# Kernel optimization log

Hardware: AMD Instinct MI355X
Metric: run time of the kernel (lower is better)

The kernel has to match this reference:

```python
import jax, jax.numpy as jnp
import numpy as np

N, E, B = 100000, 1600000, 64
TD, VD, AD = 768, 2048, 512
HC, H = 32, 4
NV, NA = 20000, 20000


def setup_inputs() -> dict:
    key = jax.random.key(0)
    ks = iter(jax.random.split(key, 80))
    def nrm(shape, scale=0.05):
        return (jax.random.normal(next(ks), shape, jnp.float32) * scale)
    inp = {}
    inp["x"] = jax.random.normal(next(ks), (N, TD), jnp.float32)
    inp["x_vision"] = jax.random.normal(next(ks), (NV, VD), jnp.float32)
    inp["x_audio"] = jax.random.normal(next(ks), (NA, AD), jnp.float32)
    inp["src"] = jax.random.randint(next(ks), (E,), 0, N, jnp.int32)
    inp["dst"] = jax.random.randint(next(ks), (E,), 0, N, jnp.int32)
    inp["vidx"] = jnp.arange(NV, dtype=jnp.int32) + 1000   # disjoint vision node ids
    inp["aidx"] = jnp.arange(NA, dtype=jnp.int32) + 30000  # disjoint audio node ids
    inp["ptr"] = (jnp.arange(B + 1) * (N // B)).astype(jnp.int32)
    # modality projections
    inp["Wt"] = nrm((HC, TD)); inp["bt"] = jnp.zeros((HC,), jnp.float32)
    inp["Wv"] = nrm((HC, VD)); inp["bv"] = jnp.zeros((HC,), jnp.float32)
    inp["gv"] = jnp.ones((HC,), jnp.float32); inp["bev"] = jnp.zeros((HC,), jnp.float32)
    inp["Wa"] = nrm((HC, AD)); inp["ba"] = jnp.zeros((HC,), jnp.float32)
    inp["ga"] = jnp.ones((HC,), jnp.float32); inp["bea"] = jnp.zeros((HC,), jnp.float32)
    # GATv2 convs: (in_dim, heads, concat)
    for p, cin, h, concat in (("c1", HC, H, True), ("c2", HC * H, H, True), ("c3", HC * H, H, True), ("c4", HC * H, 1, False)):
        inp[p + "_Wl"] = nrm((h * HC, cin)); inp[p + "_bl"] = jnp.zeros((h * HC,), jnp.float32)
        inp[p + "_Wr"] = nrm((h * HC, cin)); inp[p + "_br"] = jnp.zeros((h * HC,), jnp.float32)
        inp[p + "_att"] = nrm((h, HC))
        inp[p + "_b"] = jnp.zeros((h * HC if concat else HC,), jnp.float32)
    # layer norms
    for p, d in (("n1", HC * H), ("n2", HC * H), ("n3", HC * H), ("n4", HC)):
        inp[p + "_g"] = jnp.ones((d,), jnp.float32); inp[p + "_b"] = jnp.zeros((d,), jnp.float32)
    inp["Wo"] = nrm((1, HC), 0.01); inp["bo"] = jnp.zeros((1,), jnp.float32)
    return inp


def layernorm(x, g, b):
    m = x.mean(-1, keepdims=True)
    v = x.var(-1, keepdims=True)
    return (x - m) / jnp.sqrt(v + 1e-5) * g + b


def gatv2(x, src, dst, Wl, bl, Wr, br, att, b, concat):
    # PyG GATv2Conv (share_weights=False): e = att . leaky_relu(xl[src] + xr[dst])
    n = x.shape[0]
    h, c = att.shape
    xl = (x @ Wl.T + bl).reshape(n, h, c)
    xr = (x @ Wr.T + br).reshape(n, h, c)
    e = jnp.einsum('ehc,hc->eh', jax.nn.leaky_relu(xl[src] + xr[dst], 0.2), att)
    m = jax.ops.segment_max(e, dst, num_segments=n)          # segment softmax over dst
    w = jnp.exp(e - m[dst])
    s = jax.ops.segment_sum(w, dst, num_segments=n)
    alpha = w / (s[dst] + 1e-16)
    out = jax.ops.segment_sum(alpha[:, :, None] * xl[src], dst, num_segments=n)
    out = out.reshape(n, h * c) if concat else out.mean(1)
    return out + b


def reference(x, x_vision, x_audio, Wt, bt, Wv, bv, gv, bev, Wa, ba, ga, bea,
              c1_Wl, c1_bl, c1_Wr, c1_br, c1_att, c1_b,
              c2_Wl, c2_bl, c2_Wr, c2_br, c2_att, c2_b,
              c3_Wl, c3_bl, c3_Wr, c3_br, c3_att, c3_b,
              c4_Wl, c4_bl, c4_Wr, c4_br, c4_att, c4_b,
              n1_g, n1_b, n2_g, n2_b, n3_g, n3_b, n4_g, n4_b, Wo, bo,
              src, dst, vidx, aidx, ptr):
    n = x.shape[0]
    sl = jnp.arange(n, dtype=src.dtype)  # add_self_loops=True
    s2 = jnp.concatenate([src, sl]); d2 = jnp.concatenate([dst, sl])
    fx = x @ Wt.T + bt  # text projection (dropout = identity in eval)
    hv = jax.nn.relu(layernorm(x_vision @ Wv.T + bv, gv, bev))
    fx = fx.at[vidx].set(hv * x[vidx].mean(1, keepdims=True))
    ha = jax.nn.relu(layernorm(x_audio @ Wa.T + ba, ga, bea))
    fx = fx.at[aidx].set(ha * x[aidx].mean(1, keepdims=True))
    h1 = jax.nn.elu(layernorm(gatv2(fx, s2, d2, c1_Wl, c1_bl, c1_Wr, c1_br, c1_att, c1_b, True), n1_g, n1_b))
    h2 = jax.nn.elu(layernorm(gatv2(h1, s2, d2, c2_Wl, c2_bl, c2_Wr, c2_br, c2_att, c2_b, True) + h1, n2_g, n2_b))
    h3 = jax.nn.elu(layernorm(gatv2(h2, s2, d2, c3_Wl, c3_bl, c3_Wr, c3_br, c3_att, c3_b, True) + h2, n3_g, n3_b))
    h4 = layernorm(gatv2(h3, s2, d2, c4_Wl, c4_bl, c4_Wr, c4_br, c4_att, c4_b, False), n4_g, n4_b)
    summary = h4[ptr[:-1]]  # summary node = first node of each graph
    out = (summary @ Wo.T + bo).squeeze(-1)  # num_classes==2 -> squeeze
    return out
```

## Files before the change

kernel.cpp:

```cpp
#include <hip/hip_runtime.h>
#include <math.h>

#define NND 100000
#define NED 1600000
#define TDIM 768
#define VDIM 2048
#define ADIM 512
#define NVV 20000
#define NAA 20000
#define NBB 64
#define SUBROWS 8192

#define NBLK_N ((NND + 255) / 256)
#define NBLK_E ((NED + 255) / 256)
#define NSCAN ((NND + 1023) / 1024)
#define NPACK 576
#define NTB_TXT (NND / 32)
#define NTB_VIS (NVV / 32)
#define NTB_AUD (NAA / 32)

static __device__ __forceinline__ unsigned short f2bf(float f) {
  unsigned int u = __float_as_uint(f);
  unsigned int r = (u + 0x7fffu + ((u >> 16) & 1u)) >> 16;
  return (unsigned short)r;
}
static __device__ __forceinline__ float bf2f(unsigned int s) {
  return __uint_as_float(s << 16);
}

typedef __attribute__((ext_vector_type(8))) short bfrag;
typedef __attribute__((ext_vector_type(4))) float facc4;

static __device__ __forceinline__ bfrag pack8(const float4& a, const float4& b) {
  union { bfrag v; unsigned short u[8]; } r;
  r.u[0] = f2bf(a.x); r.u[1] = f2bf(a.y); r.u[2] = f2bf(a.z); r.u[3] = f2bf(a.w);
  r.u[4] = f2bf(b.x); r.u[5] = f2bf(b.y); r.u[6] = f2bf(b.z); r.u[7] = f2bf(b.w);
  return r.v;
}

static __device__ __forceinline__ float red16(float v) {
  #pragma unroll
  for (int m = 8; m >= 1; m >>= 1) v += __shfl_xor(v, m, 64);
  return v;
}
static __device__ __forceinline__ float red32(float v) {
  #pragma unroll
  for (int m = 16; m >= 1; m >>= 1) v += __shfl_xor(v, m, 64);
  return v;
}

__global__ void k_init(int* cnt, int* fill, int* m3, int* m2, int* cnts, int* agg, int n) {
  int i = blockIdx.x * 256 + threadIdx.x;
  if (i < n) { cnt[i] = 1; fill[i] = 1; m3[i] = 0; m2[i] = 0; }
  if (i < 2) cnts[i] = 0;
  if (i < 128) agg[i] = 0;
}

__global__ void k_cntpack(
    const int* __restrict__ dst, int* cnt,
    const float* __restrict__ W0l, const float* __restrict__ W0r, unsigned short* o0,
    const float* __restrict__ W1l, const float* __restrict__ W1r, unsigned short* o1,
    const float* __restrict__ W2l, const float* __restrict__ W2r, unsigned short* o2,
    const float* __restrict__ W3l, const float* __restrict__ W3r, unsigned short* o3,
    const float* __restrict__ Wt, unsigned short* ot,
    const float* __restrict__ Wv, unsigned short* ov,
    const float* __restrict__ Wa, unsigned short* oa) {
  int bid = blockIdx.x;
  if (bid < NBLK_E) {
    int i = bid * 256 + threadIdx.x;
    if (i < NED) atomicAdd(&cnt[dst[i]], 1);
    return;
  }
  int i = (bid - NBLK_E) * 256 + threadIdx.x;
  if (i < 4096) { o0[i] = f2bf(W0l[i]); o0[4096 + i] = f2bf(W0r[i]); return; }
  i -= 4096;
  if (i < 16384) { o1[i] = f2bf(W1l[i]); o1[16384 + i] = f2bf(W1r[i]); return; }
  i -= 16384;
  if (i < 16384) { o2[i] = f2bf(W2l[i]); o2[16384 + i] = f2bf(W2r[i]); return; }
  i -= 16384;
  if (i < 4096) { o3[i] = f2bf(W3l[i]); o3[4096 + i] = f2bf(W3r[i]); return; }
  i -= 4096;
  if (i < 24576) { ot[i] = f2bf(Wt[i]); return; }
  i -= 24576;
  if (i < 65536) { ov[i] = f2bf(Wv[i]); return; }
  i -= 65536;
  if (i < 16384) { oa[i] = f2bf(Wa[i]); return; }
}

__global__ void k_scanall(const int* __restrict__ cnt, int* rp, int* agg, int n) {
  __shared__ int lds[256];
  int t = threadIdx.x, b = blockIdx.x;
  int base = b * 1024;
  int v[4];
  int s = 0;
  #pragma unroll
  for (int j = 0; j < 4; ++j) {
    int i = base + t * 4 + j;
    int c = (i < n) ? cnt[i] : 0;
    s += c; v[j] = s;
  }
  lds[t] = s;
  __syncthreads();
  for (int ofs = 1; ofs < 256; ofs <<= 1) {
    int x = (t >= ofs) ? lds[t - ofs] : 0;
    __syncthreads();
    lds[t] += x;
    __syncthreads();
  }
  int excl = (t > 0) ? lds[t - 1] : 0;
  int total = lds[255];
  if (t == 0) atomicExch(&agg[b], total);
  __syncthreads();
  int psum = 0;
  for (int j = t; j < b; j += 256) {
    int a;
    do { a = atomicAdd(&agg[j], 0); } while (a == 0);
    psum += a;
  }
  lds[t] = psum;
  __syncthreads();
  for (int ofs = 128; ofs >= 1; ofs >>= 1) {
    if (t < ofs) lds[t] += lds[t + ofs];
    __syncthreads();
  }
  int prefix = lds[0];
  #pragma unroll
  for (int j = 0; j < 4; ++j) {
    int i = base + t * 4 + j;
    if (i < n) rp[i + 1] = prefix + excl + v[j];
  }
  if (b == 0 && t == 0) rp[0] = 0;
}

__global__ void k_fill(const int* __restrict__ src, const int* __restrict__ dst,
                       const int* __restrict__ rp, int* fill, int* colidx, int n, int e) {
  int i = blockIdx.x * 256 + threadIdx.x;
  if (i < n) colidx[rp[i]] = i;
  if (i < e) {
    int d = dst[i];
    int p = atomicAdd(&fill[d], 1);
    colidx[rp[d] + p] = src[i];
  }
}

__global__ void k_prep4m(const int* __restrict__ ptr, const int* __restrict__ rp,
                         const int* __restrict__ colidx, int* off, int* gidx, int* mark3) {
  if (blockIdx.x > 0) {
    int node = ptr[blockIdx.x - 1];
    int eb = rp[node], ee = rp[node + 1];
    if (threadIdx.x == 0) mark3[node] = 1;
    for (int e = eb + (int)threadIdx.x; e < ee; e += 256) mark3[colidx[e]] = 1;
    return;
  }
  __shared__ int cnt_s[64];
  __shared__ int off_s[65];
  int t = threadIdx.x;
  if (t < 64) {
    int node = ptr[t];
    int deg = rp[node + 1] - rp[node];
    if (deg > 126) deg = 126;
    cnt_s[t] = deg + 1;
  }
  __syncthreads();
  if (t == 0) {
    int acc = 0;
    for (int i = 0; i < 64; ++i) { off_s[i] = acc; acc += cnt_s[i]; }
    off_s[64] = acc;
  }
  __syncthreads();
  if (t < 65) off[t] = off_s[t];
  if (t < 64) {
    int node = ptr[t];
    int o = off_s[t];
    gidx[o] = node;
    int eb = rp[node];
    int deg = cnt_s[t] - 1;
    for (int j = 0; j < deg; ++j) gidx[o + 1 + j] = colidx[eb + j];
  }
}

__global__ void k_mark2s(const int* __restrict__ mark3, const int* __restrict__ rp,
                         const int* __restrict__ colidx, int* mark2, int n) {
  int i = blockIdx.x * 256 + threadIdx.x;
  if (i >= n || !mark3[i]) return;
  mark2[i] = 1;
  int eb = rp[i], ee = rp[i + 1];
  for (int e = eb; e < ee; ++e) mark2[colidx[e]] = 1;
}

__global__ void k_compact2(const int* __restrict__ m3, const int* __restrict__ m2,
                           int* l3, int* l2, int* cnts, int n) {
  int i = blockIdx.x * 256 + threadIdx.x;
  if (i < n) {
    if (m3[i]) { int p = atomicAdd(&cnts[0], 1); l3[p] = i; }
    if (m2[i]) { int p = atomicAdd(&cnts[1], 1); l2[p] = i; }
  }
}

template <int K, bool MEAN, bool OBF>
static __device__ __forceinline__ void gemm_in_body(
    const float* __restrict__ A, const unsigned short* __restrict__ Wb,
    const float* __restrict__ bias, void* __restrict__ Cv,
    float* __restrict__ rowmean, int bid, float* lred) {
  constexpr int KH = K / 2;
  constexpr int KT2 = KH / 32;
  constexpr int NG = KT2 / 2;
  static_assert(KT2 % 2 == 0 && NG % 2 == 0, "need even group count");
  const int wid = (int)threadIdx.x >> 6;
  const int lane = (int)threadIdx.x & 63;
  const int tile = wid & 1;
  const int kh = wid >> 1;
  const int r16 = lane & 15;
  const int kg = lane >> 4;
  const int m0 = (bid * 2 + tile) * 16;
  const float* arow = A + (size_t)(m0 + r16) * K + kh * KH + kg * 8;
  const unsigned short* w0 = Wb + (size_t)r16 * K + kh * KH + kg * 8;
  const unsigned short* w1 = Wb + (size_t)(16 + r16) * K + kh * KH + kg * 8;

  float4 A0[4], A1[4];
  bfrag W0[4], W1[4];
  facc4 acc0 = (facc4){0.f, 0.f, 0.f, 0.f};
  facc4 acc1 = (facc4){0.f, 0.f, 0.f, 0.f};
  float msum = 0.f;

  auto loadg = [&](float4* dA, bfrag* dW, int g) {
    #pragma unroll
    for (int t = 0; t < 2; ++t) {
      const float4* ap = reinterpret_cast<const float4*>(arow + (g * 2 + t) * 32);
      dA[2 * t] = ap[0];
      dA[2 * t + 1] = ap[1];
    }
    #pragma unroll
    for (int t = 0; t < 2; ++t) {
      dW[2 * t]     = *reinterpret_cast<const bfrag*>(w0 + (g * 2 + t) * 32);
      dW[2 * t + 1] = *reinterpret_cast<const bfrag*>(w1 + (g * 2 + t) * 32);
    }
  };
  auto consume = [&](const float4* sA, const bfrag* sW) {
    #pragma unroll
    for (int t = 0; t < 2; ++t) {
      float4 a0 = sA[2 * t], a1 = sA[2 * t + 1];
      if (MEAN) msum += (a0.x + a0.y + a0.z + a0.w) + (a1.x + a1.y + a1.z + a1.w);
      bfrag af = pack8(a0, a1);
      acc0 = __builtin_amdgcn_mfma_f32_16x16x32_bf16(af, sW[2 * t], acc0, 0, 0, 0);
      acc1 = __builtin_amdgcn_mfma_f32_16x16x32_bf16(af, sW[2 * t + 1], acc1, 0, 0, 0);
    }
  };

  loadg(A0, W0, 0);
  #pragma unroll 1
  for (int g = 0; g < NG; g += 2) {
    loadg(A1, W1, g + 1);
    __builtin_amdgcn_sched_barrier(0);
    consume(A0, W0);
    if (g + 2 < NG) loadg(A0, W0, g + 2);
    __builtin_amdgcn_sched_barrier(0);
    consume(A1, W1);
  }

  float* my = lred + ((size_t)tile * 64 + lane) * 9;
  if (kh == 1) {
    #pragma unroll
    for (int r = 0; r < 4; ++r) { my[r] = acc0[r]; my[4 + r] = acc1[r]; }
    my[8] = msum;
  }
  __syncthreads();
  if (kh == 1) return;
  #pragma unroll
  for (int r = 0; r < 4; ++r) { acc0[r] += my[r]; acc1[r] += my[4 + r]; }
  if (MEAN) msum += my[8];

  float b0v = bias[r16], b1v = bias[16 + r16];
  #pragma unroll
  for (int r = 0; r < 4; ++r) {
    int rowg = m0 + kg * 4 + r;
    float v0 = acc0[r] + b0v, v1 = acc1[r] + b1v;
    if (OBF) {
      unsigned short* C = (unsigned short*)Cv;
      C[(size_t)rowg * 32 + r16] = f2bf(v0);
      C[(size_t)rowg * 32 + 16 + r16] = f2bf(v1);
    } else {
      float* C = (float*)Cv;
      C[(size_t)rowg * 32 + r16] = v0;
      C[(size_t)rowg * 32 + 16 + r16] = v1;
    }
  }
  if (MEAN) {
    msum += __shfl_xor(msum, 16, 64);
    msum += __shfl_xor(msum, 32, 64);
    if (lane < 16) rowmean[m0 + r16] = msum * (1.f / (float)K);
  }
}

__global__ __launch_bounds__(256) void k_gemm_in_all(
    const float* __restrict__ x, const unsigned short* __restrict__ wbt,
    const float* __restrict__ bt, unsigned short* fx, float* rowmean,
    const float* __restrict__ xv, const unsigned short* __restrict__ wbv,
    const float* __restrict__ bv, float* hvraw,
    const float* __restrict__ xa, const unsigned short* __restrict__ wba,
    const float* __restrict__ ba, float* haraw) {
  __shared__ float lred[2 * 64 * 9];
  int bid = blockIdx.x;
  if (bid < NTB_TXT) {
    gemm_in_body<TDIM, true, true>(x, wbt, bt, fx, rowmean, bid, lred);
  } else if (bid < NTB_TXT + NTB_VIS) {
    gemm_in_body<VDIM, false, false>(xv, wbv, bv, hvraw, nullptr, bid - NTB_TXT, lred);
  } else {
    gemm_in_body<ADIM, false, false>(xa, wba, ba, haraw, nullptr, bid - NTB_TXT - NTB_VIS, lred);
  }
}

template <int K, int NHALF, int WAVES, int MODE>
__global__ __launch_bounds__(WAVES * 64) void gemm_mfma(
    const unsigned short* __restrict__ A,
    const unsigned short* __restrict__ Wb,
    const float* __restrict__ bl, const float* __restrict__ br,
    unsigned short* __restrict__ Cl, unsigned short* __restrict__ Cr, int M,
    const int* __restrict__ rows, const int* __restrict__ rcnt) {
  constexpr int KT = K / 32;
  constexpr int NT = 2 * NHALF / 16;
  constexpr int NPW = NT / WAVES;
  static_assert(NPW >= 1, "bad wave split");
  const int wid = (int)threadIdx.x >> 6;
  const int lane = (int)threadIdx.x & 63;
  const int r16 = lane & 15;
  const int kg = lane >> 4;
  const int m0 = blockIdx.x * 16;
  int nr = M;
  if (MODE >= 1) nr = *rcnt;
  if (m0 >= nr) return;
  bfrag bf[NPW][KT];
  #pragma unroll
  for (int n = 0; n < NPW; ++n) {
    int col = (wid * NPW + n) * 16 + r16;
    #pragma unroll
    for (int kt = 0; kt < KT; ++kt)
      bf[n][kt] = *reinterpret_cast<const bfrag*>(Wb + (size_t)col * K + kt * 32 + kg * 8);
  }
  int ra = m0 + r16;
  if (MODE >= 1) { int mm = ra < nr ? ra : nr - 1; ra = rows[mm]; }
  bfrag af[KT];
  const unsigned short* arow = A + (size_t)ra * K + kg * 8;
  #pragma unroll
  for (int kt = 0; kt < KT; ++kt)
    af[kt] = *reinterpret_cast<const bfrag*>(arow + kt * 32);
  facc4 acc[NPW];
  #pragma unroll
  for (int n = 0; n < NPW; ++n) acc[n] = (facc4){0.f, 0.f, 0.f, 0.f};
  #pragma unroll
  for (int kt = 0; kt < KT; ++kt)
    #pragma unroll
    for (int n = 0; n < NPW; ++n)
      acc[n] = __builtin_amdgcn_mfma_f32_16x16x32_bf16(af[kt], bf[n][kt], acc[n], 0, 0, 0);
  #pragma unroll
  for (int n = 0; n < NPW; ++n) {
    int colg = (wid * NPW + n) * 16 + r16;
    bool isL = colg < NHALF;
    float bias = isL ? bl[colg] : br[colg - NHALF];
    #pragma unroll
    for (int r = 0; r < 4; ++r) {
      int m = m0 + kg * 4 + r;
      if (MODE == 1 && m >= nr) continue;
      int rowg = (MODE == 1) ? rows[m] : m;
      unsigned short v = f2bf(acc[n][r] + bias);
      if (isL) Cl[(size_t)rowg * NHALF + colg] = v;
      else     Cr[(size_t)rowg * NHALF + (colg - NHALF)] = v;
    }
  }
}

template <bool RES, bool WL>
__global__ __launch_bounds__(256) void gat_agg_post128(
    const unsigned short* __restrict__ xl, const unsigned short* __restrict__ xr,
    const float* __restrict__ att,
    const int* __restrict__ rp, const int* __restrict__ colidx,
    const float* __restrict__ cb, const unsigned short* res,
    const float* __restrict__ g, const float* __restrict__ b,
    unsigned short* __restrict__ out, int n,
    const int* __restrict__ wl, const int* __restrict__ wcnt) {
  int wid = (blockIdx.x * 256 + threadIdx.x) >> 6;
  int node;
  if (WL) {
    if (wid >= *wcnt) return;
    node = wl[wid];
  } else {
    if (wid >= n) return;
    node = wid;
  }
  const int base = node * 128;
  int l = threadIdx.x & 63;
  const int lh = l & 31;
  const int half = l >> 5;
  const int c4 = 4 * lh;
  float4 a = *reinterpret_cast<const float4*>(att + c4);
  uint2 xru = *reinterpret_cast<const uint2*>(xr + base + c4);
  float xr0 = bf2f(xru.x & 0xffffu), xr1 = bf2f(xru.x >> 16);
  float xr2 = bf2f(xru.y & 0xffffu), xr3 = bf2f(xru.y >> 16);
  float m_ = -1e30f, s_ = 0.f;
  float ac0 = 0.f, ac1 = 0.f, ac2 = 0.f, ac3 = 0.f;
  int eb = rp[node], ee = rp[node + 1];
  int cnt = ee - eb;
  int nstep = (cnt + 1) >> 1;

  auto step = [&](uint2 cur, bool go) {
    float x0 = bf2f(cur.x & 0xffffu), x1 = bf2f(cur.x >> 16);
    float x2 = bf2f(cur.y & 0xffffu), x3 = bf2f(cur.y >> 16);
    float z0 = x0 + xr0, z1 = x1 + xr1, z2 = x2 + xr2, z3 = x3 + xr3;
    float t = (z0 > 0.f ? z0 : 0.2f * z0) * a.x + (z1 > 0.f ? z1 : 0.2f * z1) * a.y
            + (z2 > 0.f ? z2 : 0.2f * z2) * a.z + (z3 > 0.f ? z3 : 0.2f * z3) * a.w;
    t += __shfl_xor(t, 1, 64);
    t += __shfl_xor(t, 2, 64);
    t += __shfl_xor(t, 4, 64);
    if (!go) t = -1e30f;
    if (__any(t > m_ + 4.0f)) {
      float nm = fmaxf(m_, t);
      float p = __expf(m_ - nm);
      float w = __expf(t - nm);
      s_ = s_ * p + w;
      ac0 = ac0 * p + w * x0; ac1 = ac1 * p + w * x1;
      ac2 = ac2 * p + w * x2; ac3 = ac3 * p + w * x3;
      m_ = nm;
    } else {
      float w = __expf(t - m_);
      s_ += w;
      ac0 = fmaf(w, x0, ac0); ac1 = fmaf(w, x1, ac1);
      ac2 = fmaf(w, x2, ac2); ac3 = fmaf(w, x3, ac3);
    }
  };
  auto eclamp = [&](int s) { int e = 2 * s + half; return eb + (e < cnt ? e : cnt - 1); };
  auto ldx = [&](int sn) {
    return *reinterpret_cast<const uint2*>(xl + (size_t)sn * 128 + c4);
  };

  int idx[4];
  uint2 pv[4];
  #pragma unroll
  for (int k = 0; k < 4; ++k) idx[k] = colidx[eclamp(k)];
  #pragma unroll
  for (int k = 0; k < 4; ++k) pv[k] = ldx(idx[k]);
  for (int i = 0; i < nstep; i += 4) {
    uint2 q[4];
    #pragma unroll
    for (int k = 0; k < 4; ++k) q[k] = pv[k];
    if (i + 4 < nstep) {
      #pragma unroll
      for (int k = 0; k < 4; ++k) idx[k] = colidx[eclamp(i + 4 + k)];
      #pragma unroll
      for (int k = 0; k < 4; ++k) pv[k] = ldx(idx[k]);
    }
    step(q[0], 2 * i + half < cnt);
    if (i + 1 < nstep) step(q[1], 2 * (i + 1) + half < cnt);
    if (i + 2 < nstep) step(q[2], 2 * (i + 2) + half < cnt);
    if (i + 3 < nstep) step(q[3], 2 * (i + 3) + half < cnt);
  }

  float om = __shfl_xor(m_, 32, 64);
  float os = __shfl_xor(s_, 32, 64);
  float oa0 = __shfl_xor(ac0, 32, 64);
  float oa1 = __shfl_xor(ac1, 32, 64);
  float oa2 = __shfl_xor(ac2, 32, 64);
  float oa3 = __shfl_xor(ac3, 32, 64);
  float nm = fmaxf(m_, om);
  float ps = __expf(m_ - nm), po = __expf(om - nm);
  float s = s_ * ps + os * po;
  float inv = 1.f / (s + 1e-16f);
  float4 cbv = *reinterpret_cast<const float4*>(cb + c4);
  float v0 = (ac0 * ps + oa0 * po) * inv + cbv.x;
  float v1 = (ac1 * ps + oa1 * po) * inv + cbv.y;
  float v2 = (ac2 * ps + oa2 * po) * inv + cbv.z;
  float v3 = (ac3 * ps + oa3 * po) * inv + cbv.w;
  if (RES) {
    uint2 rv = *reinterpret_cast<const uint2*>(res + base + c4);
    v0 += bf2f(rv.x & 0xffffu); v1 += bf2f(rv.x >> 16);
    v2 += bf2f(rv.y & 0xffffu); v3 += bf2f(rv.y >> 16);
  }
  float S = v0 + v1 + v2 + v3;
  float Q = v0 * v0 + v1 * v1 + v2 * v2 + v3 * v3;
  #pragma unroll
  for (int m = 16; m >= 1; m >>= 1) {
    S += __shfl_xor(S, m, 64);
    Q += __shfl_xor(Q, m, 64);
  }
  float mean = S * (1.f / 128.f);
  float var = Q * (1.f / 128.f) - mean * mean;
  float rstd = rsqrtf(var + 1e-5f);
  float4 gv = *reinterpret_cast<const float4*>(g + c4);
  float4 bv = *reinterpret_cast<const float4*>(b + c4);
  float y0 = (v0 - mean) * rstd * gv.x + bv.x;
  float y1 = (v1 - mean) * rstd * gv.y + bv.y;
  float y2 = (v2 - mean) * rstd * gv.z + bv.z;
  float y3 = (v3 - mean) * rstd * gv.w + bv.w;
  y0 = (y0 > 0.f) ? y0 : expm1f(y0);
  y1 = (y1 > 0.f) ? y1 : expm1f(y1);
  y2 = (y2 > 0.f) ? y2 : expm1f(y2);
  y3 = (y3 > 0.f) ? y3 : expm1f(y3);
  if (half == 0) {
    uint2 o;
    o.x = (unsigned int)f2bf(y0) | ((unsigned int)f2bf(y1) << 16);
    o.y = (unsigned int)f2bf(y2) | ((unsigned int)f2bf(y3) << 16);
    *reinterpret_cast<uint2*>(out + base + c4) = o;
  }
}

__global__ __launch_bounds__(256) void k_agg4_final(
    const unsigned short* __restrict__ xls, const unsigned short* __restrict__ xrs,
    const float* __restrict__ att, const int* __restrict__ off,
    const float* __restrict__ cb, const float* __restrict__ g,
    const float* __restrict__ b, const float* __restrict__ Wo,
    const float* __restrict__ bo, float* __restrict__ out) {
  int wid = (blockIdx.x * 256 + threadIdx.x) >> 6;
  int l = threadIdx.x & 63;
  int lg = l & 15;
  int node = 4 * wid + (l >> 4);
  int c2 = 2 * lg;
  int p0 = off[node], pe = off[node + 1];
  int deg = pe - p0 - 1;
  float2 a = *reinterpret_cast<const float2*>(att + c2);
  unsigned int xru = *reinterpret_cast<const unsigned int*>(xrs + (size_t)p0 * 32 + c2);
  float xr0 = bf2f(xru & 0xffffu), xr1 = bf2f(xru >> 16);
  float m_ = -1e30f, s_ = 0.f, accx = 0.f, accy = 0.f;
  for (int i = 0;; ++i) {
    bool go = i < deg;
    if (!__any(go)) break;
    float xcx = 0.f, xcy = 0.f;
    float t = -1e30f;
    if (go) {
      unsigned int pv = *reinterpret_cast<const unsigned int*>(xls + (size_t)(p0 + 1 + i) * 32 + c2);
      xcx = bf2f(pv & 0xffffu);
      xcy = bf2f(pv >> 16);
      float z0 = xcx + xr0, z1 = xcy + xr1;
      t = (z0 > 0.f ? z0 : 0.2f * z0) * a.x + (z1 > 0.f ? z1 : 0.2f * z1) * a.y;
    }
    t = red16(t);
    if (!go) t = -1e30f;
    if (__any(t > m_ + 4.0f)) {
      float nm = fmaxf(m_, t);
      float p = __expf(m_ - nm);
      float w = __expf(t - nm);
      s_ = s_ * p + w;
      accx = accx * p + w * xcx;
      accy = accy * p + w * xcy;
      m_ = nm;
    } else {
      float w = __expf(t - m_);
      s_ += w;
      accx = fmaf(w, xcx, accx);
      accy = fmaf(w, xcy, accy);
    }
  }
  float inv = 1.f / (s_ + 1e-16f);
  float2 cbv = *reinterpret_cast<const float2*>(cb + c2);
  float v0 = accx * inv + cbv.x;
  float v1 = accy * inv + cbv.y;
  float S = red16(v0 + v1);
  float Q = red16(v0 * v0 + v1 * v1);
  float mean = S * (1.f / 32.f);
  float var = Q * (1.f / 32.f) - mean * mean;
  float rstd = rsqrtf(var + 1e-5f);
  float2 gv = *reinterpret_cast<const float2*>(g + c2);
  float2 bv = *reinterpret_cast<const float2*>(b + c2);
  float y0 = (v0 - mean) * rstd * gv.x + bv.x;
  float y1 = (v1 - mean) * rstd * gv.y + bv.y;
  float2 wo = *reinterpret_cast<const float2*>(Wo + c2);
  float d = red16(y0 * wo.x + y1 * wo.y);
  if (lg == 0) out[node] = d + bo[0];
}

__global__ __launch_bounds__(256) void k_modal2(
    unsigned short* fx, const float* __restrict__ hv, const float* __restrict__ ha,
    const int* __restrict__ vidx, const int* __restrict__ aidx,
    const float* __restrict__ gv, const float* __restrict__ bev,
    const float* __restrict__ ga, const float* __restrict__ bea,
    const float* __restrict__ rowmean, int nv, int na) {
  int wid = (blockIdx.x * 256 + threadIdx.x) >> 6;
  int l = threadIdx.x & 63;
  if (wid >= nv + na) return;
  bool isV = wid < nv;
  int w2 = isV ? wid : wid - nv;
  const float* hraw = isV ? hv : ha;
  const float* gg = isV ? gv : ga;
  const float* be = isV ? bev : bea;
  int node = isV ? vidx[w2] : aidx[w2];
  float mean = rowmean[node];
  float hval = (l < 32) ? hraw[(size_t)w2 * 32 + l] : 0.f;
  float S = red32(hval);
  float Q = red32(hval * hval);
  if (l < 32) {
    float m2 = S * (1.f / 32.f);
    float var = Q * (1.f / 32.f) - m2 * m2;
    float rstd = rsqrtf(var + 1e-5f);
    float y = (hval - m2) * rstd * gg[l] + be[l];
    y = fmaxf(y, 0.f);
    fx[(size_t)node * 32 + l] = f2bf(y * mean);
  }
}

extern "C" void kernel_launch(void* const* d_in, const int* in_sizes, int n_in,
                              void* d_out, int out_size, void* d_ws, size_t ws_size,
                              hipStream_t stream) {
  const float* x   = (const float*)d_in[0];
  const float* xv  = (const float*)d_in[1];
  const float* xa  = (const float*)d_in[2];
  const int* src   = (const int*)d_in[3];
  const int* dst   = (const int*)d_in[4];
  const int* vidx  = (const int*)d_in[5];
  const int* aidx  = (const int*)d_in[6];
  const int* ptr   = (const int*)d_in[7];
  const float* Wt  = (const float*)d_in[8];
  const float* bt  = (const float*)d_in[9];
  const float* Wv  = (const float*)d_in[10];
  const float* bv  = (const float*)d_in[11];
  const float* gv  = (const float*)d_in[12];
  const float* bev = (const float*)d_in[13];
  const float* Wa  = (const float*)d_in[14];
  const float* ba  = (const float*)d_in[15];
  const float* ga  = (const float*)d_in[16];
  const float* bea = (const float*)d_in[17];
  const float* cW_l[4], *cb_l[4], *cW_r[4], *cb_r[4], *c_att[4], *c_b[4];
  for (int i = 0; i < 4; ++i) {
    cW_l[i]  = (const float*)d_in[18 + 6 * i + 0];
    cb_l[i]  = (const float*)d_in[18 + 6 * i + 1];
    cW_r[i]  = (const float*)d_in[18 + 6 * i + 2];
    cb_r[i]  = (const float*)d_in[18 + 6 * i + 3];
    c_att[i] = (const float*)d_in[18 + 6 * i + 4];
    c_b[i]   = (const float*)d_in[18 + 6 * i + 5];
  }
  const float* ng[4], *nb_[4];
  for (int i = 0; i < 4; ++i) {
    ng[i]  = (const float*)d_in[42 + 2 * i + 0];
    nb_[i] = (const float*)d_in[42 + 2 * i + 1];
  }
  const float* Wo = (const float*)d_in[50];
  const float* bo = (const float*)d_in[51];
  float* out = (float*)d_out;

  char* w = (char*)d_ws;
  auto alloc = [&](size_t bytes) {
    char* p = w;
    w += (bytes + 255) & ~(size_t)255;
    return p;
  };
  int* rowptr = (int*)alloc((NND + 1) * sizeof(int));
  int* cnt    = (int*)alloc(NND * sizeof(int));
  int* aggs   = (int*)alloc(128 * sizeof(int));
  int* colidx = (int*)alloc((size_t)(NED + NND) * sizeof(int));
  float* rowmean = (float*)alloc((size_t)NND * sizeof(float));
  unsigned short* fx = (unsigned short*)alloc((size_t)NND * 32 * sizeof(unsigned short));
  unsigned short* h  = (unsigned short*)alloc((size_t)NND * 128 * sizeof(unsigned short));
  unsigned short* xlb = (unsigned short*)alloc((size_t)NND * 128 * sizeof(unsigned short));
  unsigned short* xrb = (unsigned short*)alloc((size_t)NND * 128 * sizeof(unsigned short));
  float* hvraw = (float*)alloc((size_t)NVV * 32 * sizeof(float));
  float* haraw = (float*)alloc((size_t)NAA * 32 * sizeof(float));
  unsigned short* wb0 = (unsigned short*)alloc(256 * 32 * sizeof(unsigned short));
  unsigned short* wb1 = (unsigned short*)alloc(256 * 128 * sizeof(unsigned short));
  unsigned short* wb2 = (unsigned short*)alloc(256 * 128 * sizeof(unsigned short));
  unsigned short* wb3 = (unsigned short*)alloc(64 * 128 * sizeof(unsigned short));
  unsigned short* wbt = (unsigned short*)alloc(32 * TDIM * sizeof(unsigned short));
  unsigned short* wbv = (unsigned short*)alloc(32 * VDIM * sizeof(unsigned short));
  unsigned short* wba = (unsigned short*)alloc(32 * ADIM * sizeof(unsigned short));
  int* off4 = (int*)alloc(65 * sizeof(int));
  int* gidx = (int*)alloc(SUBROWS * sizeof(int));
  unsigned short* xls = (unsigned short*)alloc((size_t)SUBROWS * 32 * sizeof(unsigned short));
  unsigned short* xrs = (unsigned short*)alloc((size_t)SUBROWS * 32 * sizeof(unsigned short));
  int* mark3 = (int*)alloc((size_t)NND * sizeof(int));
  int* mark2 = (int*)alloc((size_t)NND * sizeof(int));
  int* list3 = (int*)alloc((size_t)NND * sizeof(int));
  int* list2 = (int*)alloc((size_t)NND * sizeof(int));
  int* cnts  = (int*)alloc(2 * sizeof(int));

  const int nwave_n = (NND * 64 + 255) / 256;
  const int nwave_m2 = ((NVV + NAA) * 64 + 255) / 256;
  const int ntile = (NND + 15) / 16;

  int* fill = list2;
  k_init<<<NBLK_N, 256, 0, stream>>>(cnt, fill, mark3, mark2, cnts, aggs, NND);
  k_cntpack<<<NBLK_E + NPACK, 256, 0, stream>>>(
      dst, cnt,
      cW_l[0], cW_r[0], wb0, cW_l[1], cW_r[1], wb1,
      cW_l[2], cW_r[2], wb2, cW_l[3], cW_r[3], wb3,
      Wt, wbt, Wv, wbv, Wa, wba);
  k_scanall<<<NSCAN, 256, 0, stream>>>(cnt, rowptr, aggs, NND);
  k_fill<<<NBLK_E, 256, 0, stream>>>(src, dst, rowptr, fill, colidx, NND, NED);
  k_prep4m<<<65, 256, 0, stream>>>(ptr, rowptr, colidx, off4, gidx, mark3);
  k_mark2s<<<NBLK_N, 256, 0, stream>>>(mark3, rowptr, colidx, mark2, NND);
  k_compact2<<<NBLK_N, 256, 0, stream>>>(mark3, mark2, list3, list2, cnts, NND);
  k_gemm_in_all<<<NTB_TXT + NTB_VIS + NTB_AUD, 256, 0, stream>>>(
      x, wbt, bt, fx, rowmean, xv, wbv, bv, hvraw, xa, wba, ba, haraw);
  k_modal2<<<nwave_m2, 256, 0, stream>>>(
      fx, hvraw, haraw, vidx, aidx, gv, bev, ga, bea, rowmean, NVV, NAA);

  gemm_mfma<32, 128, 8, 0><<<ntile, 512, 0, stream>>>(
      fx, wb0, cb_l[0], cb_r[0], xlb, xrb, NND, nullptr, nullptr);
  gat_agg_post128<false, false><<<nwave_n, 256, 0, stream>>>(
      xlb, xrb, c_att[0], rowptr, colidx, c_b[0], nullptr, ng[0], nb_[0], h, NND,
      nullptr, nullptr);

  gemm_mfma<128, 128, 8, 0><<<ntile, 512, 0, stream>>>(
      h, wb1, cb_l[1], cb_r[1], xlb, xrb, NND, nullptr, nullptr);
  gat_agg_post128<true, true><<<nwave_n, 256, 0, stream>>>(
      xlb, xrb, c_att[1], rowptr, colidx, c_b[1], h, ng[1], nb_[1], h, NND,
      list2, cnts + 1);

  gemm_mfma<128, 128, 8, 1><<<ntile, 512, 0, stream>>>(
      h, wb2, cb_l[2], cb_r[2], xlb, xrb, NND, list2, cnts + 1);
  gat_agg_post128<true, true><<<4096, 256, 0, stream>>>(
      xlb, xrb, c_att[2], rowptr, colidx, c_b[2], h, ng[2], nb_[2], h, NND,
      list3, cnts + 0);

  gemm_mfma<128, 32, 4, 2><<<SUBROWS / 16, 256, 0, stream>>>(
      h, wb3, cb_l[3], cb_r[3], xls, xrs, SUBROWS, gidx, off4 + 64);
  k_agg4_final<<<4, 256, 0, stream>>>(
      xls, xrs, c_att[3], off4, c_b[3], ng[3], nb_[3], Wo, bo, out);
}
```

Measured before the change: 618.0 us.

## Fuse independent preprocessing and compute kernels into combined launches

Merges independent stages into shared kernel launches, dispatched by block index: init with weight packing, input GEMMs with degree counting, scan with modality norm, CSR fill with the first GEMM, the first aggregation with subgraph prep, and the second GEMM with marking and compaction. The aim is to cut the number of kernel launches and let unrelated work overlap on the GPU. The first aggregation's grid is hardcoded to 25000 blocks, and the combined kernels may see lower occupancy from mixed register and LDS demands.

```diff
diff --git a/kernel.cpp b/kernel.cpp
--- a/kernel.cpp
+++ b/kernel.cpp
@@ -13,8 +13,13 @@
 
 #define NBLK_N ((NND + 255) / 256)
 #define NBLK_E ((NED + 255) / 256)
+#define NBLK_E512 ((NED + 511) / 512)
+#define NM512 ((NND + 511) / 512)
 #define NSCAN ((NND + 1023) / 1024)
 #define NPACK 576
+#define NTILE ((NND + 15) / 16)
+#define NWAVEN ((NND * 64 + 255) / 256)
+#define NWAVEM2 (((NVV + NAA) * 64 + 255) / 256)
 #define NTB_TXT (NND / 32)
 #define NTB_VIS (NVV / 32)
 #define NTB_AUD (NAA / 32)
@@ -49,15 +54,9 @@
   return v;
 }
 
-__global__ void k_init(int* cnt, int* fill, int* m3, int* m2, int* cnts, int* agg, int n) {
-  int i = blockIdx.x * 256 + threadIdx.x;
-  if (i < n) { cnt[i] = 1; fill[i] = 1; m3[i] = 0; m2[i] = 0; }
-  if (i < 2) cnts[i] = 0;
-  if (i < 128) agg[i] = 0;
-}
-
-__global__ void k_cntpack(
-    const int* __restrict__ dst, int* cnt,
+
+static __device__ __forceinline__ void pack_body(
+    int i,
     const float* __restrict__ W0l, const float* __restrict__ W0r, unsigned short* o0,
     const float* __restrict__ W1l, const float* __restrict__ W1r, unsigned short* o1,
     const float* __restrict__ W2l, const float* __restrict__ W2r, unsigned short* o2,
@@ -65,13 +64,6 @@
     const float* __restrict__ Wt, unsigned short* ot,
     const float* __restrict__ Wv, unsigned short* ov,
     const float* __restrict__ Wa, unsigned short* oa) {
-  int bid = blockIdx.x;
-  if (bid < NBLK_E) {
-    int i = bid * 256 + threadIdx.x;
-    if (i < NED) atomicAdd(&cnt[dst[i]], 1);
-    return;
-  }
-  int i = (bid - NBLK_E) * 256 + threadIdx.x;
   if (i < 4096) { o0[i] = f2bf(W0l[i]); o0[4096 + i] = f2bf(W0r[i]); return; }
   i -= 4096;
   if (i < 16384) { o1[i] = f2bf(W1l[i]); o1[16384 + i] = f2bf(W1r[i]); return; }
@@ -87,9 +79,9 @@
   if (i < 16384) { oa[i] = f2bf(Wa[i]); return; }
 }
 
-__global__ void k_scanall(const int* __restrict__ cnt, int* rp, int* agg, int n) {
-  __shared__ int lds[256];
-  int t = threadIdx.x, b = blockIdx.x;
+static __device__ __forceinline__ void scan_body(
+    const int* __restrict__ cnt, int* rp, int* agg, int n, int b, int* lds) {
+  int t = threadIdx.x;
   int base = b * 1024;
   int v[4];
   int s = 0;
@@ -132,28 +124,46 @@
   if (b == 0 && t == 0) rp[0] = 0;
 }
 
-__global__ void k_fill(const int* __restrict__ src, const int* __restrict__ dst,
-                       const int* __restrict__ rp, int* fill, int* colidx, int n, int e) {
-  int i = blockIdx.x * 256 + threadIdx.x;
-  if (i < n) colidx[rp[i]] = i;
-  if (i < e) {
-    int d = dst[i];
-    int p = atomicAdd(&fill[d], 1);
-    colidx[rp[d] + p] = src[i];
-  }
-}
-
-__global__ void k_prep4m(const int* __restrict__ ptr, const int* __restrict__ rp,
-                         const int* __restrict__ colidx, int* off, int* gidx, int* mark3) {
-  if (blockIdx.x > 0) {
-    int node = ptr[blockIdx.x - 1];
+static __device__ __forceinline__ void modal_body(
+    unsigned short* fx, const float* __restrict__ hv, const float* __restrict__ ha,
+    const int* __restrict__ vidx, const int* __restrict__ aidx,
+    const float* __restrict__ gv, const float* __restrict__ bev,
+    const float* __restrict__ ga, const float* __restrict__ bea,
+    const float* __restrict__ rowmean, int nv, int na, int bid) {
+  int wid = bid * 4 + ((int)threadIdx.x >> 6);
+  int l = threadIdx.x & 63;
+  if (wid >= nv + na) return;
+  bool isV = wid < nv;
+  int w2 = isV ? wid : wid - nv;
+  const float* hraw = isV ? hv : ha;
+  const float* gg = isV ? gv : ga;
+  const float* be = isV ? bev : bea;
+  int node = isV ? vidx[w2] : aidx[w2];
+  float mean = rowmean[node];
+  float hval = (l < 32) ? hraw[(size_t)w2 * 32 + l] : 0.f;
+  float S = red32(hval);
+  float Q = red32(hval * hval);
+  if (l < 32) {
+    float m2 = S * (1.f / 32.f);
+    float var = Q * (1.f / 32.f) - m2 * m2;
+    float rstd = rsqrtf(var + 1e-5f);
+    float y = (hval - m2) * rstd * gg[l] + be[l];
+    y = fmaxf(y, 0.f);
+    fx[(size_t)node * 32 + l] = f2bf(y * mean);
+  }
+}
+
+static __device__ __forceinline__ void prep4_body(
+    const int* __restrict__ ptr, const int* __restrict__ rp,
+    const int* __restrict__ colidx, int* off, int* gidx, int* mark3,
+    int bid, int* cnt_s, int* off_s) {
+  if (bid > 0) {
+    int node = ptr[bid - 1];
     int eb = rp[node], ee = rp[node + 1];
     if (threadIdx.x == 0) mark3[node] = 1;
     for (int e = eb + (int)threadIdx.x; e < ee; e += 256) mark3[colidx[e]] = 1;
     return;
   }
-  __shared__ int cnt_s[64];
-  __shared__ int off_s[65];
   int t = threadIdx.x;
   if (t < 64) {
     int node = ptr[t];
@@ -176,24 +186,6 @@
     int eb = rp[node];
     int deg = cnt_s[t] - 1;
     for (int j = 0; j < deg; ++j) gidx[o + 1 + j] = colidx[eb + j];
-  }
-}
-
-__global__ void k_mark2s(const int* __restrict__ mark3, const int* __restrict__ rp,
-                         const int* __restrict__ colidx, int* mark2, int n) {
-  int i = blockIdx.x * 256 + threadIdx.x;
-  if (i >= n || !mark3[i]) return;
-  mark2[i] = 1;
-  int eb = rp[i], ee = rp[i + 1];
-  for (int e = eb; e < ee; ++e) mark2[colidx[e]] = 1;
-}
-
-__global__ void k_compact2(const int* __restrict__ m3, const int* __restrict__ m2,
-                           int* l3, int* l2, int* cnts, int n) {
-  int i = blockIdx.x * 256 + threadIdx.x;
-  if (i < n) {
-    if (m3[i]) { int p = atomicAdd(&cnts[0], 1); l3[p] = i; }
-    if (m2[i]) { int p = atomicAdd(&cnts[1], 1); l2[p] = i; }
   }
 }
 
@@ -292,31 +284,13 @@
   }
 }
 
-__global__ __launch_bounds__(256) void k_gemm_in_all(
-    const float* __restrict__ x, const unsigned short* __restrict__ wbt,
-    const float* __restrict__ bt, unsigned short* fx, float* rowmean,
-    const float* __restrict__ xv, const unsigned short* __restrict__ wbv,
-    const float* __restrict__ bv, float* hvraw,
-    const float* __restrict__ xa, const unsigned short* __restrict__ wba,
-    const float* __restrict__ ba, float* haraw) {
-  __shared__ float lred[2 * 64 * 9];
-  int bid = blockIdx.x;
-  if (bid < NTB_TXT) {
-    gemm_in_body<TDIM, true, true>(x, wbt, bt, fx, rowmean, bid, lred);
-  } else if (bid < NTB_TXT + NTB_VIS) {
-    gemm_in_body<VDIM, false, false>(xv, wbv, bv, hvraw, nullptr, bid - NTB_TXT, lred);
-  } else {
-    gemm_in_body<ADIM, false, false>(xa, wba, ba, haraw, nullptr, bid - NTB_TXT - NTB_VIS, lred);
-  }
-}
-
 template <int K, int NHALF, int WAVES, int MODE>
-__global__ __launch_bounds__(WAVES * 64) void gemm_mfma(
+static __device__ __forceinline__ void gemm_body(
     const unsigned short* __restrict__ A,
     const unsigned short* __restrict__ Wb,
     const float* __restrict__ bl, const float* __restrict__ br,
     unsigned short* __restrict__ Cl, unsigned short* __restrict__ Cr, int M,
-    const int* __restrict__ rows, const int* __restrict__ rcnt) {
+    const int* __restrict__ rows, const int* __restrict__ rcnt, int bid) {
   constexpr int KT = K / 32;
   constexpr int NT = 2 * NHALF / 16;
   constexpr int NPW = NT / WAVES;
@@ -325,7 +299,7 @@
   const int lane = (int)threadIdx.x & 63;
   const int r16 = lane & 15;
   const int kg = lane >> 4;
-  const int m0 = blockIdx.x * 16;
+  const int m0 = bid * 16;
   int nr = M;
   if (MODE >= 1) nr = *rcnt;
   if (m0 >= nr) return;
@@ -370,15 +344,15 @@
 }
 
 template <bool RES, bool WL>
-__global__ __launch_bounds__(256) void gat_agg_post128(
+static __device__ __forceinline__ void agg_body(
     const unsigned short* __restrict__ xl, const unsigned short* __restrict__ xr,
     const float* __restrict__ att,
     const int* __restrict__ rp, const int* __restrict__ colidx,
     const float* __restrict__ cb, const unsigned short* res,
     const float* __restrict__ g, const float* __restrict__ b,
     unsigned short* __restrict__ out, int n,
-    const int* __restrict__ wl, const int* __restrict__ wcnt) {
-  int wid = (blockIdx.x * 256 + threadIdx.x) >> 6;
+    const int* __restrict__ wl, const int* __restrict__ wcnt, int bid) {
+  int wid = bid * 4 + ((int)threadIdx.x >> 6);
   int node;
   if (WL) {
     if (wid >= *wcnt) return;
@@ -500,6 +474,166 @@
     o.y = (unsigned int)f2bf(y2) | ((unsigned int)f2bf(y3) << 16);
     *reinterpret_cast<uint2*>(out + base + c4) = o;
   }
+}
+
+
+__global__ __launch_bounds__(256) void k_initpack(
+    int* cnt, int* fill, int* m3, int* m2, int* cnts, int* agg,
+    const float* __restrict__ W0l, const float* __restrict__ W0r, unsigned short* o0,
+    const float* __restrict__ W1l, const float* __restrict__ W1r, unsigned short* o1,
+    const float* __restrict__ W2l, const float* __restrict__ W2r, unsigned short* o2,
+    const float* __restrict__ W3l, const float* __restrict__ W3r, unsigned short* o3,
+    const float* __restrict__ Wt, unsigned short* ot,
+    const float* __restrict__ Wv, unsigned short* ov,
+    const float* __restrict__ Wa, unsigned short* oa) {
+  int bid = blockIdx.x;
+  if (bid < NBLK_N) {
+    int i = bid * 256 + threadIdx.x;
+    if (i < NND) { cnt[i] = 1; fill[i] = 1; m3[i] = 0; m2[i] = 0; }
+    if (i < 2) cnts[i] = 0;
+    if (i < 128) agg[i] = 0;
+    return;
+  }
+  pack_body((bid - NBLK_N) * 256 + threadIdx.x,
+            W0l, W0r, o0, W1l, W1r, o1, W2l, W2r, o2, W3l, W3r, o3,
+            Wt, ot, Wv, ov, Wa, oa);
+}
+
+__global__ __launch_bounds__(256) void k_gin_count(
+    const float* __restrict__ x, const unsigned short* __restrict__ wbt,
+    const float* __restrict__ bt, unsigned short* fx, float* rowmean,
+    const float* __restrict__ xv, const unsigned short* __restrict__ wbv,
+    const float* __restrict__ bv, float* hvraw,
+    const float* __restrict__ xa, const unsigned short* __restrict__ wba,
+    const float* __restrict__ ba, float* haraw,
+    const int* __restrict__ dst, int* cnt) {
+  __shared__ float lred[2 * 64 * 9];
+  int bid = blockIdx.x;
+  if (bid < NTB_TXT) {
+    gemm_in_body<TDIM, true, true>(x, wbt, bt, fx, rowmean, bid, lred);
+    return;
+  }
+  bid -= NTB_TXT;
+  if (bid < NTB_VIS) {
+    gemm_in_body<VDIM, false, false>(xv, wbv, bv, hvraw, nullptr, bid, lred);
+    return;
+  }
+  bid -= NTB_VIS;
+  if (bid < NTB_AUD) {
+    gemm_in_body<ADIM, false, false>(xa, wba, ba, haraw, nullptr, bid, lred);
+    return;
+  }
+  bid -= NTB_AUD;
+  int i = bid * 256 + threadIdx.x;
+  if (i < NED) atomicAdd(&cnt[dst[i]], 1);
+}
+
+__global__ __launch_bounds__(256) void k_scan_modal(
+    const int* __restrict__ cnt, int* rp, int* agg,
+    unsigned short* fx, const float* __restrict__ hv, const float* __restrict__ ha,
+    const int* __restrict__ vidx, const int* __restrict__ aidx,
+    const float* __restrict__ gv, const float* __restrict__ bev,
+    const float* __restrict__ ga, const float* __restrict__ bea,
+    const float* __restrict__ rowmean) {
+  __shared__ int lds[256];
+  int bid = blockIdx.x;
+  if (bid < NSCAN) {
+    scan_body(cnt, rp, agg, NND, bid, lds);
+    return;
+  }
+  modal_body(fx, hv, ha, vidx, aidx, gv, bev, ga, bea, rowmean, NVV, NAA, bid - NSCAN);
+}
+
+__global__ __launch_bounds__(512) void k_fill_gemm1(
+    const unsigned short* __restrict__ fx, const unsigned short* __restrict__ wb0,
+    const float* __restrict__ bl, const float* __restrict__ br,
+    unsigned short* __restrict__ xlb, unsigned short* __restrict__ xrb,
+    const int* __restrict__ src, const int* __restrict__ dst,
+    const int* __restrict__ rp, int* fill, int* colidx) {
+  int bid = blockIdx.x;
+  if (bid < NTILE) {
+    gemm_body<32, 128, 8, 0>(fx, wb0, bl, br, xlb, xrb, NND, nullptr, nullptr, bid);
+    return;
+  }
+  int i = (bid - NTILE) * 512 + threadIdx.x;
+  if (i < NND) colidx[rp[i]] = i;
+  if (i < NED) {
+    int d = dst[i];
+    int p = atomicAdd(&fill[d], 1);
+    colidx[rp[d] + p] = src[i];
+  }
+}
+
+__global__ __launch_bounds__(256) void k_agg1_prep(
+    const unsigned short* __restrict__ xlb, const unsigned short* __restrict__ xrb,
+    const float* __restrict__ att, const int* __restrict__ rp,
+    const int* __restrict__ colidx, const float* __restrict__ cb,
+    const float* __restrict__ g, const float* __restrict__ b,
+    unsigned short* __restrict__ h,
+    const int* __restrict__ ptr, int* off, int* gidx, int* mark3) {
+  __shared__ int cnt_s[64];
+  __shared__ int off_s[65];
+  int bid = blockIdx.x;
+  if (bid < NWAVEN / 4 * 4 / 4) {}
+  if (bid < 25000) {
+    agg_body<false, false>(xlb, xrb, att, rp, colidx, cb, nullptr, g, b, h, NND,
+                           nullptr, nullptr, bid);
+    return;
+  }
+  prep4_body(ptr, rp, colidx, off, gidx, mark3, bid - 25000, cnt_s, off_s);
+}
+
+__global__ __launch_bounds__(512) void k_gemm2_mark(
+    const unsigned short* __restrict__ h, const unsigned short* __restrict__ wb1,
+    const float* __restrict__ bl, const float* __restrict__ br,
+    unsigned short* __restrict__ xlb, unsigned short* __restrict__ xrb,
+    const int* __restrict__ mark3, int* mark2,
+    const int* __restrict__ rp, const int* __restrict__ colidx,
+    int* list3, int* cnts) {
+  int bid = blockIdx.x;
+  if (bid < NTILE) {
+    gemm_body<128, 128, 8, 0>(h, wb1, bl, br, xlb, xrb, NND, nullptr, nullptr, bid);
+    return;
+  }
+  bid -= NTILE;
+  if (bid < NM512) {
+    int i = bid * 512 + threadIdx.x;
+    if (i < NND && mark3[i]) {
+      mark2[i] = 1;
+      int eb = rp[i], ee = rp[i + 1];
+      for (int e = eb; e < ee; ++e) mark2[colidx[e]] = 1;
+    }
+    return;
+  }
+  bid -= NM512;
+  int i = bid * 512 + threadIdx.x;
+  if (i < NND && mark3[i]) { int p = atomicAdd(&cnts[0], 1); list3[p] = i; }
+}
+
+__global__ __launch_bounds__(256) void k_compact1(
+    const int* __restrict__ m2, int* l2, int* cnt, int n) {
+  int i = blockIdx.x * 256 + threadIdx.x;
+  if (i < n && m2[i]) { int p = atomicAdd(cnt, 1); l2[p] = i; }
+}
+
+template <int K, int NHALF, int WAVES, int MODE>
+__global__ __launch_bounds__(WAVES * 64) void gemm_mfma(
+    const unsigned short* __restrict__ A, const unsigned short* __restrict__ Wb,
+    const float* __restrict__ bl, const float* __restrict__ br,
+    unsigned short* __restrict__ Cl, unsigned short* __restrict__ Cr, int M,
+    const int* __restrict__ rows, const int* __restrict__ rcnt) {
+  gemm_body<K, NHALF, WAVES, MODE>(A, Wb, bl, br, Cl, Cr, M, rows, rcnt, blockIdx.x);
+}
+
+template <bool RES, bool WL>
+__global__ __launch_bounds__(256) void gat_agg_post128(
+    const unsigned short* __restrict__ xl, const unsigned short* __restrict__ xr,
+    const float* __restrict__ att, const int* __restrict__ rp,
+    const int* __restrict__ colidx, const float* __restrict__ cb,
+    const unsigned short* res, const float* __restrict__ g,
+    const float* __restrict__ b, unsigned short* __restrict__ out, int n,
+    const int* __restrict__ wl, const int* __restrict__ wcnt) {
+  agg_body<RES, WL>(xl, xr, att, rp, colidx, cb, res, g, b, out, n, wl, wcnt, blockIdx.x);
 }
 
 __global__ __launch_bounds__(256) void k_agg4_final(
@@ -564,35 +698,6 @@
   float2 wo = *reinterpret_cast<const float2*>(Wo + c2);
   float d = red16(y0 * wo.x + y1 * wo.y);
   if (lg == 0) out[node] = d + bo[0];
-}
-
-__global__ __launch_bounds__(256) void k_modal2(
-    unsigned short* fx, const float* __restrict__ hv, const float* __restrict__ ha,
-    const int* __restrict__ vidx, const int* __restrict__ aidx,
-    const float* __restrict__ gv, const float* __restrict__ bev,
-    const float* __restrict__ ga, const float* __restrict__ bea,
-    const float* __restrict__ rowmean, int nv, int na) {
-  int wid = (blockIdx.x * 256 + threadIdx.x) >> 6;
-  int l = threadIdx.x & 63;
-  if (wid >= nv + na) return;
-  bool isV = wid < nv;
-  int w2 = isV ? wid : wid - nv;
-  const float* hraw = isV ? hv : ha;
-  const float* gg = isV ? gv : ga;
-  const float* be = isV ? bev : bea;
-  int node = isV ? vidx[w2] : aidx[w2];
-  float mean = rowmean[node];
-  float hval = (l < 32) ? hraw[(size_t)w2 * 32 + l] : 0.f;
-  float S = red32(hval);
-  float Q = red32(hval * hval);
-  if (l < 32) {
-    float m2 = S * (1.f / 32.f);
-    float var = Q * (1.f / 32.f) - m2 * m2;
-    float rstd = rsqrtf(var + 1e-5f);
-    float y = (hval - m2) * rstd * gg[l] + be[l];
-    y = fmaxf(y, 0.f);
-    fx[(size_t)node * 32 + l] = f2bf(y * mean);
-  }
 }
 
 extern "C" void kernel_launch(void* const* d_in, const int* in_sizes, int n_in,
@@ -668,45 +773,33 @@
   int* list2 = (int*)alloc((size_t)NND * sizeof(int));
   int* cnts  = (int*)alloc(2 * sizeof(int));
 
-  const int nwave_n = (NND * 64 + 255) / 256;
-  const int nwave_m2 = ((NVV + NAA) * 64 + 255) / 256;
-  const int ntile = (NND + 15) / 16;
-
   int* fill = list2;
-  k_init<<<NBLK_N, 256, 0, stream>>>(cnt, fill, mark3, mark2, cnts, aggs, NND);
-  k_cntpack<<<NBLK_E + NPACK, 256, 0, stream>>>(
-      dst, cnt,
+
+  k_initpack<<<NBLK_N + NPACK, 256, 0, stream>>>(
+      cnt, fill, mark3, mark2, cnts, aggs,
       cW_l[0], cW_r[0], wb0, cW_l[1], cW_r[1], wb1,
       cW_l[2], cW_r[2], wb2, cW_l[3], cW_r[3], wb3,
       Wt, wbt, Wv, wbv, Wa, wba);
-  k_scanall<<<NSCAN, 256, 0, stream>>>(cnt, rowptr, aggs, NND);
-  k_fill<<<NBLK_E, 256, 0, stream>>>(src, dst, rowptr, fill, colidx, NND, NED);
-  k_prep4m<<<65, 256, 0, stream>>>(ptr, rowptr, colidx, off4, gidx, mark3);
-  k_mark2s<<<NBLK_N, 256, 0, stream>>>(mark3, rowptr, colidx, mark2, NND);
-  k_compact2<<<NBLK_N, 256, 0, stream>>>(mark3, mark2, list3, list2, cnts, NND);
-  k_gemm_in_all<<<NTB_TXT + NTB_VIS + NTB_AUD, 256, 0, stream>>>(
-      x, wbt, bt, fx, rowmean, xv, wbv, bv, hvraw, xa, wba, ba, haraw);
-  k_modal2<<<nwave_m2, 256, 0, stream>>>(
-      fx, hvraw, haraw, vidx, aidx, gv, bev, ga, bea, rowmean, NVV, NAA);
-
-  gemm_mfma<32, 128, 8, 0><<<ntile, 512, 0, stream>>>(
-      fx, wb0, cb_l[0], cb_r[0], xlb, xrb, NND, nullptr, nullptr);
-  gat_agg_post128<false, false><<<nwave_n, 256, 0, stream>>>(
-      xlb, xrb, c_att[0], rowptr, colidx, c_b[0], nullptr, ng[0], nb_[0], h, NND,
-      nullptr, nullptr);
-
-  gemm_mfma<128, 128, 8, 0><<<ntile, 512, 0, stream>>>(
-      h, wb1, cb_l[1], cb_r[1], xlb, xrb, NND, nullptr, nullptr);
-  gat_agg_post128<true, true><<<nwave_n, 256, 0, stream>>>(
+  k_gin_count<<<NTB_TXT + NTB_VIS + NTB_AUD + NBLK_E, 256, 0, stream>>>(
+      x, wbt, bt, fx, rowmean, xv, wbv, bv, hvraw, xa, wba, ba, haraw, dst, cnt);
+  k_scan_modal<<<NSCAN + NWAVEM2, 256, 0, stream>>>(
+      cnt, rowptr, aggs, fx, hvraw, haraw, vidx, aidx, gv, bev, ga, bea, rowmean);
+  k_fill_gemm1<<<NTILE + NBLK_E512, 512, 0, stream>>>(
+      fx, wb0, cb_l[0], cb_r[0], xlb, xrb, src, dst, rowptr, fill, colidx);
+  k_agg1_prep<<<25000 + 65, 256, 0, stream>>>(
+      xlb, xrb, c_att[0], rowptr, colidx, c_b[0], ng[0], nb_[0], h,
+      ptr, off4, gidx, mark3);
+  k_gemm2_mark<<<NTILE + NM512 + NM512, 512, 0, stream>>>(
+      h, wb1, cb_l[1], cb_r[1], xlb, xrb, mark3, mark2, rowptr, colidx, list3, cnts);
+  k_compact1<<<NBLK_N, 256, 0, stream>>>(mark2, list2, cnts + 1, NND);
+  gat_agg_post128<true, true><<<NWAVEN, 256, 0, stream>>>(
       xlb, xrb, c_att[1], rowptr, colidx, c_b[1], h, ng[1], nb_[1], h, NND,
       list2, cnts + 1);
-
-  gemm_mfma<128, 128, 8, 1><<<ntile, 512, 0, stream>>>(
+  gemm_mfma<128, 128, 8, 1><<<NTILE, 512, 0, stream>>>(
       h, wb2, cb_l[2], cb_r[2], xlb, xrb, NND, list2, cnts + 1);
   gat_agg_post128<true, true><<<4096, 256, 0, stream>>>(
       xlb, xrb, c_att[2], rowptr, colidx, c_b[2], h, ng[2], nb_[2], h, NND,
       list3, cnts + 0);
-
   gemm_mfma<128, 32, 4, 2><<<SUBROWS / 16, 256, 0, stream>>>(
       h, wb3, cb_l[3], cb_r[3], xls, xrs, SUBROWS, gidx, off4 + 64);
   k_agg4_final<<<4, 256, 0, stream>>>(
```

Measured after the change: 582.5 us. -5.7%, faster.
